# Optimization experiments

Measured on AMD Instinct MI355X. Metric: run time of the kernel, lower is better.

Reference implementation:

```python
import jax, jax.numpy as jnp
import numpy as np

# Model dims (from ModelArgs defaults)
B, S, DIM = 1, 1024, 2880
H, HKV, HD = 64, 8, 64        # query heads, kv heads, head dim
GROUP = H // HKV              # 8 query heads per kv head
WINDOW = 128                  # sliding window (layer_idx=0 -> active)
THETA = 150000.0


def setup_inputs() -> dict:
    key = jax.random.key(0)
    ks = jax.random.split(key, 10)
    rn = lambda k, shape, sc: (jax.random.normal(k, shape, jnp.float32) * sc)
    return {
        "x": rn(ks[0], (B, S, DIM), 1.0),
        "wq_w": rn(ks[1], (H * HD, DIM), 0.02),
        "wq_b": rn(ks[2], (H * HD,), 0.02),
        "wk_w": rn(ks[3], (HKV * HD, DIM), 0.02),
        "wk_b": rn(ks[4], (HKV * HD,), 0.02),
        "wv_w": rn(ks[5], (HKV * HD, DIM), 0.02),
        "wv_b": rn(ks[6], (HKV * HD,), 0.02),
        "wo_w": rn(ks[7], (DIM, H * HD), 0.02),
        "wo_b": rn(ks[8], (DIM,), 0.02),
        "sinks": rn(ks[9], (H,), 1.0),
    }


def _rope(t):
    # t: [B, S, h, HD]; half-split (rotate_half) RoPE with base THETA
    half = HD // 2
    inv_freq = 1.0 / (THETA ** (jnp.arange(half, dtype=jnp.float32) * 2.0 / HD))
    ang = jnp.arange(S, dtype=jnp.float32)[:, None] * inv_freq      # [S, half]
    cos = jnp.cos(ang)[None, :, None, :]
    sin = jnp.sin(ang)[None, :, None, :]
    t1, t2 = t[..., :half], t[..., half:]
    return jnp.concatenate([t1 * cos - t2 * sin, t1 * sin + t2 * cos], axis=-1)


def reference(x, wq_w, wq_b, wk_w, wk_b, wv_w, wv_b, wo_w, wo_b, sinks):
    # Projections (nn.Linear: y = x @ W^T + b)
    q = (jnp.einsum('bsd,ed->bse', x, wq_w) + wq_b).reshape(B, S, H, HD)
    k = (jnp.einsum('bsd,ed->bse', x, wk_w) + wk_b).reshape(B, S, HKV, HD)
    v = (jnp.einsum('bsd,ed->bse', x, wv_w) + wv_b).reshape(B, S, HKV, HD)

    q = _rope(q)
    k = _rope(k)

    # GQA: expand kv heads to match query heads
    k = jnp.repeat(k, GROUP, axis=2)   # [B, S, H, HD]
    v = jnp.repeat(v, GROUP, axis=2)

    scale = HD ** -0.5
    scores = jnp.einsum('bihd,bjhd->bhij', q, k) * scale   # [B, H, S, S]

    # Causal + sliding-window mask: attend to j with 0 <= i-j < WINDOW
    i = jnp.arange(S)[:, None]
    j = jnp.arange(S)[None, :]
    allowed = (j <= i) & ((i - j) < WINDOW)
    scores = jnp.where(allowed, scores, jnp.float32(-1e30))

    # Softmax with per-head learnable sink logit folded into normalization
    sink = sinks[None, :, None, None]                       # [1, H, 1, 1]
    m = jnp.maximum(jnp.max(scores, axis=-1, keepdims=True), sink)
    e = jnp.exp(scores - m)
    denom = jnp.sum(e, axis=-1, keepdims=True) + jnp.exp(sink - m)
    probs = e / denom                                       # sink mass dropped

    out = jnp.einsum('bhij,bjhd->bihd', probs, v).reshape(B, S, H * HD)
    return jnp.einsum('bse,de->bsd', out, wo_w) + wo_b
```

## Files before the change

kernel.cpp:

```cpp
#include <hip/hip_runtime.h>

typedef __attribute__((ext_vector_type(4))) float f32x4;
typedef __attribute__((ext_vector_type(8))) short s16x8;
typedef unsigned short u16;

#define DEVI __device__ __forceinline__

DEVI u16 f2bf(float f) {
    union { float f; unsigned int u; } v; v.f = f;
    unsigned int r = v.u + 0x7FFFu + ((v.u >> 16) & 1u);
    return (u16)(r >> 16);
}
DEVI float bf2f(u16 b) {
    union { unsigned int u; float f; } v; v.u = ((unsigned int)b) << 16;
    return v.f;
}

typedef __attribute__((address_space(1))) void gv_t;
typedef __attribute__((address_space(3))) void sv_t;

#define GLOAD16(SRC, DST) __builtin_amdgcn_global_load_lds( \
    (gv_t*)(SRC), (sv_t*)(DST), 16, 0, 0)

DEVI f32x4 mfma_bf16(s16x8 a, s16x8 b, f32x4 c) {
    return __builtin_amdgcn_mfma_f32_16x16x32_bf16(a, b, c, 0, 0, 0);
}

__global__ void cvt1_kernel(
    const float* __restrict__ x,  const float* __restrict__ wq, const float* __restrict__ wk,
    const float* __restrict__ wv,
    u16* __restrict__ xb, u16* __restrict__ wqb, u16* __restrict__ wkb,
    u16* __restrict__ wvb)
{
    int id = blockIdx.x * 256 + threadIdx.x;
    const float* s; u16* d; int off;
    if      (id < 737280)  { s = x;  d = xb;  off = id; }
    else if (id < 3686400) { s = wq; d = wqb; off = id - 737280; }
    else if (id < 4055040) { s = wk; d = wkb; off = id - 3686400; }
    else                   { s = wv; d = wvb; off = id - 4055040; }
    f32x4 v = *(const f32x4*)(s + (size_t)off * 4);
    union { u16 u[4]; unsigned long long ll; } o;
    #pragma unroll
    for (int j = 0; j < 4; ++j) o.u[j] = f2bf(v[j]);
    *(unsigned long long*)(d + (size_t)off * 4) = o.ll;
}

__global__ __launch_bounds__(256, 3) void gemm_m97(
    const u16* __restrict__ A, int lda, int kit, int ntot, int gemmx,
    const u16* __restrict__ W0, int t0, int n0, int c0,
    const u16* __restrict__ W1, int t1, int n1, int c1,
    const u16* __restrict__ W2, int t2, int n2, int c2,
    u16* __restrict__ C, int ldc, long long cstride,
    const float* __restrict__ cvsrc, u16* __restrict__ cvdst, int cvblk)
{
    __shared__ u16 Als[128 * 64];
    __shared__ u16 Bls[128 * 64];

    const int lin = blockIdx.x;
    const int z   = blockIdx.z;

    if (lin >= gemmx) {
        if (z == 0 && cvblk > 0) {
            const int cb_  = lin - gemmx;
            const int step = cvblk * 256;
            int idx = cb_ * 256 + threadIdx.x;
            #pragma unroll 4
            for (int i = 0; i < 16; ++i) {
                f32x4 v = *(const f32x4*)(cvsrc + (size_t)idx * 4);
                union { u16 u[4]; unsigned long long ll; } o;
                #pragma unroll
                for (int j = 0; j < 4; ++j) o.u[j] = f2bf(v[j]);
                *(unsigned long long*)(cvdst + (size_t)idx * 4) = o.ll;
                idx += step;
            }
        }
        return;
    }

    const int xc  = lin & 7;
    const int mm  = lin >> 3;
    const int nbl = xc + 8 * (mm >> 3);
    const int yt  = mm & 7;
    if (nbl >= ntot) return;

    const int tid  = threadIdx.x;
    const int lane = tid & 63;
    const int wid  = tid >> 6;
    const int li   = lane & 15;
    const int lg   = lane >> 4;
    const int m0   = yt * 128;

    const u16* W; int nt0, nsz, cb;
    if (nbl < t0)           { W = W0; nt0 = nbl * 128;             nsz = n0; cb = c0; }
    else if (nbl < t0 + t1) { W = W1; nt0 = (nbl - t0) * 128;      nsz = n1; cb = c1; }
    else                    { W = W2; nt0 = (nbl - t0 - t1) * 128; nsz = n2; cb = c2; }

    const int S  = gridDim.z;
    const int it0 = (z * kit) / S;
    const int it1 = ((z + 1) * kit) / S;
    u16* Cp = C + (long long)z * cstride;

    const int wm = (wid >> 1) * 64;
    const int wn = (wid & 1) * 64;

    f32x4 acc[4][4];
    #pragma unroll
    for (int mi = 0; mi < 4; ++mi)
        #pragma unroll
        for (int ni = 0; ni < 4; ++ni)
            acc[mi][ni] = (f32x4){0.f, 0.f, 0.f, 0.f};

    const int srow = tid >> 3;
    const int slc  = (tid & 7) ^ (srow & 7);

    for (int it = it0; it < it1; ++it) {
        const int k0 = it * 64;
        #pragma unroll
        for (int s_ = 0; s_ < 4; ++s_) {
            const u16* sa = A + (size_t)(m0 + s_ * 32 + srow) * lda + k0 + slc * 8;
            GLOAD16(sa, &Als[(s_ * 256 + tid) * 8]);
        }
        #pragma unroll
        for (int s_ = 0; s_ < 4; ++s_) {
            int wr = nt0 + s_ * 32 + srow;
            if (wr > nsz - 1) wr = nsz - 1;
            const u16* sb = W + (size_t)wr * lda + k0 + slc * 8;
            GLOAD16(sb, &Bls[(s_ * 256 + tid) * 8]);
        }
        __syncthreads();

        s16x8 af[4][2], bfv[4][2];
        #pragma unroll
        for (int mi = 0; mi < 4; ++mi)
            #pragma unroll
            for (int kc = 0; kc < 2; ++kc) {
                int row = wm + mi * 16 + li;
                int ch  = (kc * 4 + lg) ^ (row & 7);
                af[mi][kc] = *(const s16x8*)&Als[row * 64 + ch * 8];
            }
        #pragma unroll
        for (int ni = 0; ni < 4; ++ni)
            #pragma unroll
            for (int kc = 0; kc < 2; ++kc) {
                int row = wn + ni * 16 + li;
                int ch  = (kc * 4 + lg) ^ (row & 7);
                bfv[ni][kc] = *(const s16x8*)&Bls[row * 64 + ch * 8];
            }
        #pragma unroll
        for (int mi = 0; mi < 4; ++mi)
            #pragma unroll
            for (int ni = 0; ni < 4; ++ni)
                #pragma unroll
                for (int kc = 0; kc < 2; ++kc)
                    acc[mi][ni] = mfma_bf16(af[mi][kc], bfv[ni][kc], acc[mi][ni]);
        __syncthreads();
    }

    #pragma unroll
    for (int ni = 0; ni < 4; ++ni) {
        int colr = nt0 + wn + ni * 16 + li;
        if (colr < nsz) {
            #pragma unroll
            for (int mi = 0; mi < 4; ++mi)
                #pragma unroll
                for (int r = 0; r < 4; ++r) {
                    int row = m0 + wm + mi * 16 + lg * 4 + r;
                    Cp[(size_t)row * ldc + cb + colr] = f2bf(acc[mi][ni][r]);
                }
        }
    }
}

__global__ void rope_kernel(const u16* __restrict__ qkvp,
                            const float* __restrict__ qb, const float* __restrict__ kb,
                            const float* __restrict__ vb,
                            u16* __restrict__ qo, u16* __restrict__ ko, u16* __restrict__ vt)
{
    const long long PST = 1024LL * 5120;
    int id = blockIdx.x * 256 + threadIdx.x;
    int s  = id / 352;
    int g  = id % 352;
    const u16* r0 = qkvp + (size_t)s * 5120;

    if (g < 288) {
        bool isq = g < 256;
        int gg   = isq ? g : g - 256;
        int hh   = gg >> 2;
        int dg   = gg & 3;
        int col0 = (isq ? 0 : 4096) + hh * 64 + dg * 8;
        int bcol = isq ? col0 : col0 - 4096;
        const float* bias = isq ? qb : kb;

        float t1[8], t2[8];
        #pragma unroll
        for (int e = 0; e < 8; ++e) { t1[e] = bias[bcol + e]; t2[e] = bias[bcol + 32 + e]; }
        #pragma unroll
        for (int p = 0; p < 3; ++p) {
            s16x8 lo = *(const s16x8*)(r0 + col0 + p * PST);
            s16x8 hi = *(const s16x8*)(r0 + col0 + 32 + p * PST);
            #pragma unroll
            for (int e = 0; e < 8; ++e) {
                t1[e] += bf2f((u16)lo[e]);
                t2[e] += bf2f((u16)hi[e]);
            }
        }
        float sc = isq ? 0.125f : 1.0f;
        s16x8 o1, o2;
        #pragma unroll
        for (int e = 0; e < 8; ++e) {
            int d = dg * 8 + e;
            float ang = (float)s * exp2f((float)d * -0.5373314f);
            float sn, cs;
            sincosf(ang, &sn, &cs);
            o1[e] = (short)f2bf((t1[e] * cs - t2[e] * sn) * sc);
            o2[e] = (short)f2bf((t1[e] * sn + t2[e] * cs) * sc);
        }
        u16* dst = isq ? qo : ko;
        int ldd  = isq ? 4096 : 512;
        *(s16x8*)(dst + (size_t)s * ldd + bcol)      = o1;
        *(s16x8*)(dst + (size_t)s * ldd + bcol + 32) = o2;
    } else {
        int gg   = g - 288;
        int col0 = 4608 + gg * 8;
        float t[8];
        #pragma unroll
        for (int e = 0; e < 8; ++e) t[e] = vb[gg * 8 + e];
        #pragma unroll
        for (int p = 0; p < 3; ++p) {
            s16x8 v = *(const s16x8*)(r0 + col0 + p * PST);
            #pragma unroll
            for (int e = 0; e < 8; ++e) t[e] += bf2f((u16)v[e]);
        }
        #pragma unroll
        for (int e = 0; e < 8; ++e)
            vt[((size_t)(gg * 8 + e)) * 1024 + s] = f2bf(t[e]);
    }
}

__global__ void reduce_out_kernel(const u16* __restrict__ parts,
                                  const float* __restrict__ bias,
                                  float* __restrict__ out)
{
    int id = blockIdx.x * 256 + threadIdx.x;
    const long long stride = 1024LL * 2880;
    long long base = (long long)id * 8;
    float s[8];
    #pragma unroll
    for (int j = 0; j < 8; ++j) s[j] = 0.f;
    #pragma unroll
    for (int p = 0; p < 5; ++p) {
        s16x8 v = *(const s16x8*)(parts + p * stride + base);
        #pragma unroll
        for (int j = 0; j < 8; ++j) s[j] += bf2f((u16)v[j]);
    }
    int cb = (int)(base % 2880);
    f32x4 b0 = *(const f32x4*)(bias + cb);
    f32x4 b1 = *(const f32x4*)(bias + cb + 4);
    f32x4 o0 = {s[0] + b0[0], s[1] + b0[1], s[2] + b0[2], s[3] + b0[3]};
    f32x4 o1 = {s[4] + b1[0], s[5] + b1[1], s[6] + b1[2], s[7] + b1[3]};
    *(f32x4*)(out + base)     = o0;
    *(f32x4*)(out + base + 4) = o1;
}

__global__ __launch_bounds__(256, 2) void attn_kernel(
    const u16* __restrict__ Q, const u16* __restrict__ Kb, const u16* __restrict__ VT,
    const float* __restrict__ sinks, u16* __restrict__ Ob)
{
    __shared__ u16 Kls[64 * 64];
    __shared__ u16 Pls[4][16 * 72];

    const int h    = blockIdx.x;
    const int qblk = blockIdx.y;
    const int kvh  = h >> 3;
    const int tid  = threadIdx.x;
    const int lane = tid & 63;
    const int w    = tid >> 6;
    const int li   = lane & 15;
    const int lg   = lane >> 4;
    const int qw   = qblk * 64 + w * 16;

    s16x8 aq[2];
    {
        const u16* qrow = Q + ((size_t)(qw + li) * 64 + h) * 64 + lg * 8;
        aq[0] = *(const s16x8*)(qrow);
        aq[1] = *(const s16x8*)(qrow + 32);
    }

    const float snk = sinks[h];
    float m_run[4], l_run[4];
    f32x4 oacc[4];
    #pragma unroll
    for (int r = 0; r < 4; ++r) { m_run[r] = snk; l_run[r] = 1.0f; }
    #pragma unroll
    for (int ni = 0; ni < 4; ++ni) oacc[ni] = (f32x4){0.f, 0.f, 0.f, 0.f};

    const int srow = tid >> 3;
    const int slc  = (tid & 7) ^ (srow & 7);

    for (int t = 0; t < 3; ++t) {
        int jt = qblk - 2 + t;
        if (jt < 0) continue;
        int j0 = jt * 64;

        #pragma unroll
        for (int it = 0; it < 2; ++it) {
            const u16* src = Kb + ((size_t)(j0 + it * 32 + srow) * 8 + kvh) * 64 + slc * 8;
            GLOAD16(src, &Kls[(it * 256 + w * 64) * 8]);
        }

        s16x8 bv[2][4];
        #pragma unroll
        for (int kc = 0; kc < 2; ++kc)
            #pragma unroll
            for (int ni = 0; ni < 4; ++ni)
                bv[kc][ni] = *(const s16x8*)(VT +
                    ((size_t)(kvh * 64 + ni * 16 + li)) * 1024 + j0 + kc * 32 + lg * 8);

        __syncthreads();

        f32x4 sc[4];
        #pragma unroll
        for (int nf = 0; nf < 4; ++nf) {
            sc[nf] = (f32x4){0.f, 0.f, 0.f, 0.f};
            #pragma unroll
            for (int kc = 0; kc < 2; ++kc) {
                int row = nf * 16 + li;
                int ch  = (kc * 4 + lg) ^ (row & 7);
                s16x8 bk = *(const s16x8*)&Kls[row * 64 + ch * 8];
                sc[nf] = mfma_bf16(aq[kc], bk, sc[nf]);
            }
        }

        #pragma unroll
        for (int r = 0; r < 4; ++r) {
            const int qg = qw + lg * 4 + r;
            float mx = -1e30f;
            #pragma unroll
            for (int nf = 0; nf < 4; ++nf) {
                int jg = j0 + nf * 16 + li;
                bool ok = (jg <= qg) && (qg - jg < 128);
                float v = ok ? sc[nf][r] : -1e30f;
                sc[nf][r] = v;
                mx = fmaxf(mx, v);
            }
            #pragma unroll
            for (int off = 1; off < 16; off <<= 1)
                mx = fmaxf(mx, __shfl_xor(mx, off));
            float mnew = fmaxf(m_run[r], mx);
            float corr = __expf(m_run[r] - mnew);
            m_run[r] = mnew;
            float rs = 0.f;
            #pragma unroll
            for (int nf = 0; nf < 4; ++nf) {
                float p = __expf(sc[nf][r] - mnew);
                rs += p;
                Pls[w][(lg * 4 + r) * 72 + nf * 16 + li] = f2bf(p);
            }
            #pragma unroll
            for (int off = 1; off < 16; off <<= 1)
                rs += __shfl_xor(rs, off);
            l_run[r] = l_run[r] * corr + rs;
            #pragma unroll
            for (int ni = 0; ni < 4; ++ni) oacc[ni][r] *= corr;
        }
        __syncthreads();

        #pragma unroll
        for (int kc = 0; kc < 2; ++kc) {
            s16x8 pa = *(const s16x8*)&Pls[w][li * 72 + kc * 32 + lg * 8];
            #pragma unroll
            for (int ni = 0; ni < 4; ++ni)
                oacc[ni] = mfma_bf16(pa, bv[kc][ni], oacc[ni]);
        }
    }

    #pragma unroll
    for (int r = 0; r < 4; ++r) {
        float inv = 1.0f / l_run[r];
        #pragma unroll
        for (int ni = 0; ni < 4; ++ni)
            Ob[((size_t)(qw + lg * 4 + r) * 64 + h) * 64 + ni * 16 + li] = f2bf(oacc[ni][r] * inv);
    }
}

extern "C" void kernel_launch(void* const* d_in, const int* in_sizes, int n_in,
                              void* d_out, int out_size, void* d_ws, size_t ws_size,
                              hipStream_t stream)
{
    const float* x     = (const float*)d_in[0];
    const float* wq_w  = (const float*)d_in[1];
    const float* wq_b  = (const float*)d_in[2];
    const float* wk_w  = (const float*)d_in[3];
    const float* wk_b  = (const float*)d_in[4];
    const float* wv_w  = (const float*)d_in[5];
    const float* wv_b  = (const float*)d_in[6];
    const float* wo_w  = (const float*)d_in[7];
    const float* wo_b  = (const float*)d_in[8];
    const float* sinks = (const float*)d_in[9];

    char* ws = (char*)d_ws;
    u16*   xb   = (u16*)(ws + 0);
    u16*   wqb  = (u16*)(ws + 5898240ULL);
    u16*   wkb  = (u16*)(ws + 29491200ULL);
    u16*   wvb  = (u16*)(ws + 32440320ULL);
    u16*   qkvp = (u16*)(ws + 35389440ULL);
    u16*   qr   = (u16*)(ws + 0);
    u16*   kr   = (u16*)(ws + 8388608ULL);
    u16*   vt   = (u16*)(ws + 9437184ULL);
    u16*   attb = (u16*)(ws + 10485760ULL);
    u16*   oprt = (u16*)(ws + 58982400ULL);
    u16*   wob  = (u16*)(ws + 88473600ULL);

    (void)in_sizes; (void)n_in; (void)out_size; (void)ws_size;

    cvt1_kernel<<<17280, 256, 0, stream>>>(x, wq_w, wk_w, wv_w, xb, wqb, wkb, wvb);
    gemm_m97<<<dim3(1040, 1, 3), 256, 0, stream>>>(xb, 2880, 45, 40, 320,
        wqb, 32, 4096, 0,
        wkb, 4, 512, 4096,
        wvb, 4, 512, 4608,
        qkvp, 5120, 1024LL * 5120,
        wo_w, wob, 720);
    rope_kernel<<<1408, 256, 0, stream>>>(qkvp, wq_b, wk_b, wv_b, qr, kr, vt);
    attn_kernel<<<dim3(64, 16), 256, 0, stream>>>(qr, kr, vt, sinks, attb);
    gemm_m97<<<dim3(192, 1, 5), 256, 0, stream>>>(attb, 4096, 64, 23, 192,
        wob, 23, 2880, 0,
        wob, 0, 0, 0,
        wob, 0, 0, 0,
        oprt, 2880, 1024LL * 2880,
        (const float*)nullptr, (u16*)nullptr, 0);
    reduce_out_kernel<<<1440, 256, 0, stream>>>(oprt, wo_b, (float*)d_out);
}
```

Baseline: 131.8 us.

## Widen GEMM tiles to 128x256 with per-wave 128x64 output and new block ordering

Changes the bf16 MFMA GEMM from 128x128 tiles with 2x2 waves to 128x256 tiles where each of 4 waves covers all 128 rows and 64 columns. A-fragments are loaded per mi inside the loop. Block ordering is remapped so groups of blocks share N tiles across the 8 M tiles. This doubles accumulator registers to 128 floats per lane and lowers launch bounds to 2 blocks/CU, aiming for higher arithmetic intensity per LDS load. The trade-offs are fewer blocks (160 and 96 GEMM blocks) and lower occupancy.

```diff
diff --git a/kernel.cpp b/kernel.cpp
--- a/kernel.cpp
+++ b/kernel.cpp
@@ -45,8 +45,8 @@
     *(unsigned long long*)(d + (size_t)off * 4) = o.ll;
 }
 
-__global__ __launch_bounds__(256, 3) void gemm_m97(
-    const u16* __restrict__ A, int lda, int kit, int ntot, int gemmx,
+__global__ __launch_bounds__(256, 2) void gemm_w64(
+    const u16* __restrict__ A, int lda, int kit, int cpx, int gemmx,
     const u16* __restrict__ W0, int t0, int n0, int c0,
     const u16* __restrict__ W1, int t1, int n1, int c1,
     const u16* __restrict__ W2, int t2, int n2, int c2,
@@ -54,7 +54,7 @@
     const float* __restrict__ cvsrc, u16* __restrict__ cvdst, int cvblk)
 {
     __shared__ u16 Als[128 * 64];
-    __shared__ u16 Bls[128 * 64];
+    __shared__ u16 Bls[256 * 64];
 
     const int lin = blockIdx.x;
     const int z   = blockIdx.z;
@@ -77,11 +77,9 @@
         return;
     }
 
-    const int xc  = lin & 7;
-    const int mm  = lin >> 3;
-    const int nbl = xc + 8 * (mm >> 3);
-    const int yt  = mm & 7;
-    if (nbl >= ntot) return;
+    const int ord = (lin & 7) * cpx + (lin >> 3);
+    const int nbl = ord >> 3;
+    const int yt  = ord & 7;
 
     const int tid  = threadIdx.x;
     const int lane = tid & 63;
@@ -89,55 +87,46 @@
     const int li   = lane & 15;
     const int lg   = lane >> 4;
     const int m0   = yt * 128;
+    const int wn   = wid * 64;
 
     const u16* W; int nt0, nsz, cb;
-    if (nbl < t0)           { W = W0; nt0 = nbl * 128;             nsz = n0; cb = c0; }
-    else if (nbl < t0 + t1) { W = W1; nt0 = (nbl - t0) * 128;      nsz = n1; cb = c1; }
-    else                    { W = W2; nt0 = (nbl - t0 - t1) * 128; nsz = n2; cb = c2; }
+    if (nbl < t0)           { W = W0; nt0 = nbl * 256;             nsz = n0; cb = c0; }
+    else if (nbl < t0 + t1) { W = W1; nt0 = (nbl - t0) * 256;      nsz = n1; cb = c1; }
+    else                    { W = W2; nt0 = (nbl - t0 - t1) * 256; nsz = n2; cb = c2; }
 
     const int S  = gridDim.z;
     const int it0 = (z * kit) / S;
     const int it1 = ((z + 1) * kit) / S;
     u16* Cp = C + (long long)z * cstride;
 
-    const int wm = (wid >> 1) * 64;
-    const int wn = (wid & 1) * 64;
-
-    f32x4 acc[4][4];
-    #pragma unroll
-    for (int mi = 0; mi < 4; ++mi)
+    f32x4 acc[8][4];
+    #pragma unroll
+    for (int mi = 0; mi < 8; ++mi)
         #pragma unroll
         for (int ni = 0; ni < 4; ++ni)
             acc[mi][ni] = (f32x4){0.f, 0.f, 0.f, 0.f};
 
-    const int srow = tid >> 3;
-    const int slc  = (tid & 7) ^ (srow & 7);
-
     for (int it = it0; it < it1; ++it) {
         const int k0 = it * 64;
         #pragma unroll
-        for (int s_ = 0; s_ < 4; ++s_) {
-            const u16* sa = A + (size_t)(m0 + s_ * 32 + srow) * lda + k0 + slc * 8;
-            GLOAD16(sa, &Als[(s_ * 256 + tid) * 8]);
-        }
-        #pragma unroll
-        for (int s_ = 0; s_ < 4; ++s_) {
-            int wr = nt0 + s_ * 32 + srow;
+        for (int j = 0; j < 4; ++j) {
+            int g   = j * 256 + tid;
+            int row = g >> 3;
+            int cs  = (g & 7) ^ (row & 7);
+            GLOAD16(A + (size_t)(m0 + row) * lda + k0 + cs * 8, &Als[g * 8]);
+        }
+        #pragma unroll
+        for (int j = 0; j < 8; ++j) {
+            int g   = j * 256 + tid;
+            int row = g >> 3;
+            int wr  = nt0 + row;
             if (wr > nsz - 1) wr = nsz - 1;
-            const u16* sb = W + (size_t)wr * lda + k0 + slc * 8;
-            GLOAD16(sb, &Bls[(s_ * 256 + tid) * 8]);
+            int cs  = (g & 7) ^ (row & 7);
+            GLOAD16(W + (size_t)wr * lda + k0 + cs * 8, &Bls[g * 8]);
         }
         __syncthreads();
 
-        s16x8 af[4][2], bfv[4][2];
-        #pragma unroll
-        for (int mi = 0; mi < 4; ++mi)
-            #pragma unroll
-            for (int kc = 0; kc < 2; ++kc) {
-                int row = wm + mi * 16 + li;
-                int ch  = (kc * 4 + lg) ^ (row & 7);
-                af[mi][kc] = *(const s16x8*)&Als[row * 64 + ch * 8];
-            }
+        s16x8 bfv[4][2];
         #pragma unroll
         for (int ni = 0; ni < 4; ++ni)
             #pragma unroll
@@ -147,12 +136,20 @@
                 bfv[ni][kc] = *(const s16x8*)&Bls[row * 64 + ch * 8];
             }
         #pragma unroll
-        for (int mi = 0; mi < 4; ++mi)
+        for (int mi = 0; mi < 8; ++mi) {
+            s16x8 af[2];
+            #pragma unroll
+            for (int kc = 0; kc < 2; ++kc) {
+                int row = mi * 16 + li;
+                int ch  = (kc * 4 + lg) ^ (row & 7);
+                af[kc] = *(const s16x8*)&Als[row * 64 + ch * 8];
+            }
             #pragma unroll
             for (int ni = 0; ni < 4; ++ni)
                 #pragma unroll
                 for (int kc = 0; kc < 2; ++kc)
-                    acc[mi][ni] = mfma_bf16(af[mi][kc], bfv[ni][kc], acc[mi][ni]);
+                    acc[mi][ni] = mfma_bf16(af[kc], bfv[ni][kc], acc[mi][ni]);
+        }
         __syncthreads();
     }
 
@@ -161,10 +158,10 @@
         int colr = nt0 + wn + ni * 16 + li;
         if (colr < nsz) {
             #pragma unroll
-            for (int mi = 0; mi < 4; ++mi)
+            for (int mi = 0; mi < 8; ++mi)
                 #pragma unroll
                 for (int r = 0; r < 4; ++r) {
-                    int row = m0 + wm + mi * 16 + lg * 4 + r;
+                    int row = m0 + mi * 16 + lg * 4 + r;
                     Cp[(size_t)row * ldc + cb + colr] = f2bf(acc[mi][ni][r]);
                 }
         }
@@ -414,16 +411,16 @@
     (void)in_sizes; (void)n_in; (void)out_size; (void)ws_size;
 
     cvt1_kernel<<<17280, 256, 0, stream>>>(x, wq_w, wk_w, wv_w, xb, wqb, wkb, wvb);
-    gemm_m97<<<dim3(1040, 1, 3), 256, 0, stream>>>(xb, 2880, 45, 40, 320,
-        wqb, 32, 4096, 0,
-        wkb, 4, 512, 4096,
-        wvb, 4, 512, 4608,
+    gemm_w64<<<dim3(880, 1, 3), 256, 0, stream>>>(xb, 2880, 45, 20, 160,
+        wqb, 16, 4096, 0,
+        wkb, 2, 512, 4096,
+        wvb, 2, 512, 4608,
         qkvp, 5120, 1024LL * 5120,
         wo_w, wob, 720);
     rope_kernel<<<1408, 256, 0, stream>>>(qkvp, wq_b, wk_b, wv_b, qr, kr, vt);
     attn_kernel<<<dim3(64, 16), 256, 0, stream>>>(qr, kr, vt, sinks, attb);
-    gemm_m97<<<dim3(192, 1, 5), 256, 0, stream>>>(attb, 4096, 64, 23, 192,
-        wob, 23, 2880, 0,
+    gemm_w64<<<dim3(96, 1, 5), 256, 0, stream>>>(attb, 4096, 64, 12, 96,
+        wob, 12, 2880, 0,
         wob, 0, 0, 0,
         wob, 0, 0, 0,
         oprt, 2880, 1024LL * 2880,
```

Result: no change. 131.7 us (-0.1%).

## Process two query tiles per attention block, move wo conversion into attention launch

Applied to the files above, without the earlier changes.

The attention kernel now handles 128 query rows per block (two 64-row groups). Each K/V tile it loads is shared across both groups, which cuts K and V global traffic and halves the attention grid. The fp32-to-bf16 conversion of wo_w moves from the QKV GEMM launch into extra blocks of the attention launch. The output projection split-K drops from 5 to 4 parts, with the reduction adjusted to match. The tradeoffs are more registers per attention thread, fewer attention blocks to fill the GPU, and conversion blocks that now compete with attention work.

```diff
diff --git a/kernel.cpp b/kernel.cpp
--- a/kernel.cpp
+++ b/kernel.cpp
@@ -46,37 +46,16 @@
 }
 
 __global__ __launch_bounds__(256, 3) void gemm_m97(
-    const u16* __restrict__ A, int lda, int kit, int ntot, int gemmx,
+    const u16* __restrict__ A, int lda, int kit, int ntot,
     const u16* __restrict__ W0, int t0, int n0, int c0,
     const u16* __restrict__ W1, int t1, int n1, int c1,
     const u16* __restrict__ W2, int t2, int n2, int c2,
-    u16* __restrict__ C, int ldc, long long cstride,
-    const float* __restrict__ cvsrc, u16* __restrict__ cvdst, int cvblk)
+    u16* __restrict__ C, int ldc, long long cstride)
 {
     __shared__ u16 Als[128 * 64];
     __shared__ u16 Bls[128 * 64];
 
     const int lin = blockIdx.x;
-    const int z   = blockIdx.z;
-
-    if (lin >= gemmx) {
-        if (z == 0 && cvblk > 0) {
-            const int cb_  = lin - gemmx;
-            const int step = cvblk * 256;
-            int idx = cb_ * 256 + threadIdx.x;
-            #pragma unroll 4
-            for (int i = 0; i < 16; ++i) {
-                f32x4 v = *(const f32x4*)(cvsrc + (size_t)idx * 4);
-                union { u16 u[4]; unsigned long long ll; } o;
-                #pragma unroll
-                for (int j = 0; j < 4; ++j) o.u[j] = f2bf(v[j]);
-                *(unsigned long long*)(cvdst + (size_t)idx * 4) = o.ll;
-                idx += step;
-            }
-        }
-        return;
-    }
-
     const int xc  = lin & 7;
     const int mm  = lin >> 3;
     const int nbl = xc + 8 * (mm >> 3);
@@ -95,6 +74,7 @@
     else if (nbl < t0 + t1) { W = W1; nt0 = (nbl - t0) * 128;      nsz = n1; cb = c1; }
     else                    { W = W2; nt0 = (nbl - t0 - t1) * 128; nsz = n2; cb = c2; }
 
+    const int z  = blockIdx.z;
     const int S  = gridDim.z;
     const int it0 = (z * kit) / S;
     const int it1 = ((z + 1) * kit) / S;
@@ -248,7 +228,7 @@
     #pragma unroll
     for (int j = 0; j < 8; ++j) s[j] = 0.f;
     #pragma unroll
-    for (int p = 0; p < 5; ++p) {
+    for (int p = 0; p < 4; ++p) {
         s16x8 v = *(const s16x8*)(parts + p * stride + base);
         #pragma unroll
         for (int j = 0; j < 8; ++j) s[j] += bf2f((u16)v[j]);
@@ -264,41 +244,63 @@
 
 __global__ __launch_bounds__(256, 2) void attn_kernel(
     const u16* __restrict__ Q, const u16* __restrict__ Kb, const u16* __restrict__ VT,
-    const float* __restrict__ sinks, u16* __restrict__ Ob)
-{
+    const float* __restrict__ sinks, u16* __restrict__ Ob,
+    const float* __restrict__ cvsrc, u16* __restrict__ cvdst)
+{
+    if (blockIdx.x >= 64) {
+        if (blockIdx.y == 0) {
+            const int cb_  = blockIdx.x - 64;
+            const int step = 720 * 256;
+            int idx = cb_ * 256 + threadIdx.x;
+            #pragma unroll 4
+            for (int i = 0; i < 16; ++i) {
+                f32x4 v = *(const f32x4*)(cvsrc + (size_t)idx * 4);
+                union { u16 u[4]; unsigned long long ll; } o;
+                #pragma unroll
+                for (int j = 0; j < 4; ++j) o.u[j] = f2bf(v[j]);
+                *(unsigned long long*)(cvdst + (size_t)idx * 4) = o.ll;
+                idx += step;
+            }
+        }
+        return;
+    }
+
     __shared__ u16 Kls[64 * 64];
     __shared__ u16 Pls[4][16 * 72];
 
     const int h    = blockIdx.x;
-    const int qblk = blockIdx.y;
+    const int qp   = blockIdx.y;
     const int kvh  = h >> 3;
     const int tid  = threadIdx.x;
     const int lane = tid & 63;
     const int w    = tid >> 6;
     const int li   = lane & 15;
     const int lg   = lane >> 4;
-    const int qw   = qblk * 64 + w * 16;
-
-    s16x8 aq[2];
-    {
-        const u16* qrow = Q + ((size_t)(qw + li) * 64 + h) * 64 + lg * 8;
-        aq[0] = *(const s16x8*)(qrow);
-        aq[1] = *(const s16x8*)(qrow + 32);
+
+    s16x8 aq[2][2];
+    #pragma unroll
+    for (int g = 0; g < 2; ++g) {
+        const u16* qrow = Q + ((size_t)(qp * 128 + g * 64 + w * 16 + li) * 64 + h) * 64 + lg * 8;
+        aq[g][0] = *(const s16x8*)(qrow);
+        aq[g][1] = *(const s16x8*)(qrow + 32);
     }
 
     const float snk = sinks[h];
-    float m_run[4], l_run[4];
-    f32x4 oacc[4];
-    #pragma unroll
-    for (int r = 0; r < 4; ++r) { m_run[r] = snk; l_run[r] = 1.0f; }
-    #pragma unroll
-    for (int ni = 0; ni < 4; ++ni) oacc[ni] = (f32x4){0.f, 0.f, 0.f, 0.f};
+    float m_run[2][4], l_run[2][4];
+    f32x4 oacc[2][4];
+    #pragma unroll
+    for (int g = 0; g < 2; ++g) {
+        #pragma unroll
+        for (int r = 0; r < 4; ++r) { m_run[g][r] = snk; l_run[g][r] = 1.0f; }
+        #pragma unroll
+        for (int ni = 0; ni < 4; ++ni) oacc[g][ni] = (f32x4){0.f, 0.f, 0.f, 0.f};
+    }
 
     const int srow = tid >> 3;
     const int slc  = (tid & 7) ^ (srow & 7);
 
-    for (int t = 0; t < 3; ++t) {
-        int jt = qblk - 2 + t;
+    for (int t = 0; t < 4; ++t) {
+        int jt = qp * 2 - 2 + t;
         if (jt < 0) continue;
         int j0 = jt * 64;
 
@@ -318,69 +320,77 @@
 
         __syncthreads();
 
-        f32x4 sc[4];
-        #pragma unroll
-        for (int nf = 0; nf < 4; ++nf) {
-            sc[nf] = (f32x4){0.f, 0.f, 0.f, 0.f};
+        #pragma unroll
+        for (int g = 0; g < 2; ++g) {
+            if (t < g || t > g + 2) continue;
+
+            f32x4 sc[4];
+            #pragma unroll
+            for (int nf = 0; nf < 4; ++nf) {
+                sc[nf] = (f32x4){0.f, 0.f, 0.f, 0.f};
+                #pragma unroll
+                for (int kc = 0; kc < 2; ++kc) {
+                    int row = nf * 16 + li;
+                    int ch  = (kc * 4 + lg) ^ (row & 7);
+                    s16x8 bk = *(const s16x8*)&Kls[row * 64 + ch * 8];
+                    sc[nf] = mfma_bf16(aq[g][kc], bk, sc[nf]);
+                }
+            }
+
+            #pragma unroll
+            for (int r = 0; r < 4; ++r) {
+                const int qg = qp * 128 + g * 64 + w * 16 + lg * 4 + r;
+                float mx = -1e30f;
+                #pragma unroll
+                for (int nf = 0; nf < 4; ++nf) {
+                    int jg = j0 + nf * 16 + li;
+                    bool ok = (jg <= qg) && (qg - jg < 128);
+                    float v = ok ? sc[nf][r] : -1e30f;
+                    sc[nf][r] = v;
+                    mx = fmaxf(mx, v);
+                }
+                #pragma unroll
+                for (int off = 1; off < 16; off <<= 1)
+                    mx = fmaxf(mx, __shfl_xor(mx, off));
+                float mnew = fmaxf(m_run[g][r], mx);
+                float corr = __expf(m_run[g][r] - mnew);
+                m_run[g][r] = mnew;
+                float rs = 0.f;
+                #pragma unroll
+                for (int nf = 0; nf < 4; ++nf) {
+                    float p = __expf(sc[nf][r] - mnew);
+                    rs += p;
+                    Pls[w][(lg * 4 + r) * 72 + nf * 16 + li] = f2bf(p);
+                }
+                #pragma unroll
+                for (int off = 1; off < 16; off <<= 1)
+                    rs += __shfl_xor(rs, off);
+                l_run[g][r] = l_run[g][r] * corr + rs;
+                #pragma unroll
+                for (int ni = 0; ni < 4; ++ni) oacc[g][ni][r] *= corr;
+            }
+            __syncthreads();
+
             #pragma unroll
             for (int kc = 0; kc < 2; ++kc) {
-                int row = nf * 16 + li;
-                int ch  = (kc * 4 + lg) ^ (row & 7);
-                s16x8 bk = *(const s16x8*)&Kls[row * 64 + ch * 8];
-                sc[nf] = mfma_bf16(aq[kc], bk, sc[nf]);
-            }
-        }
-
+                s16x8 pa = *(const s16x8*)&Pls[w][li * 72 + kc * 32 + lg * 8];
+                #pragma unroll
+                for (int ni = 0; ni < 4; ++ni)
+                    oacc[g][ni] = mfma_bf16(pa, bv[kc][ni], oacc[g][ni]);
+            }
+        }
+    }
+
+    #pragma unroll
+    for (int g = 0; g < 2; ++g)
         #pragma unroll
         for (int r = 0; r < 4; ++r) {
-            const int qg = qw + lg * 4 + r;
-            float mx = -1e30f;
-            #pragma unroll
-            for (int nf = 0; nf < 4; ++nf) {
-                int jg = j0 + nf * 16 + li;
-                bool ok = (jg <= qg) && (qg - jg < 128);
-                float v = ok ? sc[nf][r] : -1e30f;
-                sc[nf][r] = v;
-                mx = fmaxf(mx, v);
-            }
-            #pragma unroll
-            for (int off = 1; off < 16; off <<= 1)
-                mx = fmaxf(mx, __shfl_xor(mx, off));
-            float mnew = fmaxf(m_run[r], mx);
-            float corr = __expf(m_run[r] - mnew);
-            m_run[r] = mnew;
-            float rs = 0.f;
-            #pragma unroll
-            for (int nf = 0; nf < 4; ++nf) {
-                float p = __expf(sc[nf][r] - mnew);
-                rs += p;
-                Pls[w][(lg * 4 + r) * 72 + nf * 16 + li] = f2bf(p);
-            }
-            #pragma unroll
-            for (int off = 1; off < 16; off <<= 1)
-                rs += __shfl_xor(rs, off);
-            l_run[r] = l_run[r] * corr + rs;
-            #pragma unroll
-            for (int ni = 0; ni < 4; ++ni) oacc[ni][r] *= corr;
-        }
-        __syncthreads();
-
-        #pragma unroll
-        for (int kc = 0; kc < 2; ++kc) {
-            s16x8 pa = *(const s16x8*)&Pls[w][li * 72 + kc * 32 + lg * 8];
+            float inv = 1.0f / l_run[g][r];
             #pragma unroll
             for (int ni = 0; ni < 4; ++ni)
-                oacc[ni] = mfma_bf16(pa, bv[kc][ni], oacc[ni]);
-        }
-    }
-
-    #pragma unroll
-    for (int r = 0; r < 4; ++r) {
-        float inv = 1.0f / l_run[r];
-        #pragma unroll
-        for (int ni = 0; ni < 4; ++ni)
-            Ob[((size_t)(qw + lg * 4 + r) * 64 + h) * 64 + ni * 16 + li] = f2bf(oacc[ni][r] * inv);
-    }
+                Ob[((size_t)(qp * 128 + g * 64 + w * 16 + lg * 4 + r) * 64 + h) * 64
+                   + ni * 16 + li] = f2bf(oacc[g][ni][r] * inv);
+        }
 }
 
 extern "C" void kernel_launch(void* const* d_in, const int* in_sizes, int n_in,
@@ -414,19 +424,18 @@
     (void)in_sizes; (void)n_in; (void)out_size; (void)ws_size;
 
     cvt1_kernel<<<17280, 256, 0, stream>>>(x, wq_w, wk_w, wv_w, xb, wqb, wkb, wvb);
-    gemm_m97<<<dim3(1040, 1, 3), 256, 0, stream>>>(xb, 2880, 45, 40, 320,
+    gemm_m97<<<dim3(320, 1, 3), 256, 0, stream>>>(xb, 2880, 45, 40,
         wqb, 32, 4096, 0,
         wkb, 4, 512, 4096,
         wvb, 4, 512, 4608,
-        qkvp, 5120, 1024LL * 5120,
-        wo_w, wob, 720);
+        qkvp, 5120, 1024LL * 5120);
     rope_kernel<<<1408, 256, 0, stream>>>(qkvp, wq_b, wk_b, wv_b, qr, kr, vt);
-    attn_kernel<<<dim3(64, 16), 256, 0, stream>>>(qr, kr, vt, sinks, attb);
-    gemm_m97<<<dim3(192, 1, 5), 256, 0, stream>>>(attb, 4096, 64, 23, 192,
+    attn_kernel<<<dim3(784, 8), 256, 0, stream>>>(qr, kr, vt, sinks, attb,
+                                                  wo_w, wob);
+    gemm_m97<<<dim3(192, 1, 4), 256, 0, stream>>>(attb, 4096, 64, 23,
         wob, 23, 2880, 0,
         wob, 0, 0, 0,
         wob, 0, 0, 0,
-        oprt, 2880, 1024LL * 2880,
-        (const float*)nullptr, (u16*)nullptr, 0);
+        oprt, 2880, 1024LL * 2880);
     reduce_out_kernel<<<1440, 256, 0, stream>>>(oprt, wo_b, (float*)d_out);
 }
```

Measured after the change: 136.8 us. 1.04x slower.
